# Kernel optimization log

Hardware: AMD Instinct MI355X
Metric: run time of the kernel (lower is better)

Reference implementation:

```python
import jax, jax.numpy as jnp
import numpy as np

SR = 44100.0
N_FFT = 2048
BANDS = 128
C_IN = 2
D_OUT = 128
B = 8
T = 512


def _hz_to_mel(f):
    # Slaney mel scale (librosa default, htk=False)
    f = np.asarray(f, dtype=np.float64)
    f_sp = 200.0 / 3.0
    min_log_hz = 1000.0
    min_log_mel = min_log_hz / f_sp  # 15.0
    logstep = np.log(6.4) / 27.0
    lin = f / f_sp
    log = min_log_mel + np.log(np.maximum(f, 1e-10) / min_log_hz) / logstep
    return np.where(f >= min_log_hz, log, lin)


def _mel_to_hz(m):
    m = np.asarray(m, dtype=np.float64)
    f_sp = 200.0 / 3.0
    min_log_mel = 15.0
    logstep = np.log(6.4) / 27.0
    lin = m * f_sp
    log = 1000.0 * np.exp(logstep * (m - min_log_mel))
    return np.where(m >= min_log_mel, log, lin)


def _mel_filters(sr, n_fft, n_mels):
    # librosa.filters.mel(..., norm=None, fmin=0, fmax=sr/2)
    F = n_fft // 2 + 1
    fftfreqs = np.linspace(0.0, sr / 2.0, F)
    mels = np.linspace(_hz_to_mel(0.0), _hz_to_mel(sr / 2.0), n_mels + 2)
    mel_f = _mel_to_hz(mels)
    fdiff = np.diff(mel_f)
    ramps = mel_f[:, None] - fftfreqs[None, :]
    lower = -ramps[:-2] / fdiff[:-1, None]
    upper = ramps[2:] / fdiff[1:, None]
    return np.maximum(0.0, np.minimum(lower, upper))  # (n_mels, F)


def _build_bands(sr, n_fft, bands_num):
    # Mirrors BandSplit.__init__: edge residual bands + per-band nonzero gather tables.
    F = n_fft // 2 + 1
    mb = _mel_filters(sr, n_fft, bands_num - 2)
    b0 = np.zeros(F)
    i = int(np.argmax(mb[0]))
    b0[:i] = 1.0 - mb[0, :i]
    bl = np.zeros(F)
    i = int(np.argmax(mb[-1]))
    bl[i:] = 1.0 - mb[-1, i:]
    melbanks = np.concatenate([b0[None, :], mb, bl[None, :]], axis=0)  # (K, F)
    ola = melbanks.sum(axis=0)  # (F,), ~1.0 everywhere
    idx_list = [np.nonzero(melbanks[k])[0] for k in range(bands_num)]
    W = max(len(ix) for ix in idx_list)  # max band width
    pad_idx = n_fft // 2
    idxs = np.full((bands_num, W), pad_idx, dtype=np.int32)
    vals = np.zeros((bands_num, W), dtype=np.float32)
    for k, ix in enumerate(idx_list):
        idxs[k, : len(ix)] = ix
        vals[k, : len(ix)] = melbanks[k, ix]
    mask = (vals != 0.0).astype(np.float32)
    return (idxs.reshape(-1), vals.reshape(-1), mask.reshape(-1),
            ola.astype(np.float32), W)


def setup_inputs() -> dict:
    key = jax.random.key(0)
    k_x, k_w1, k_b1, k_w2, k_b2 = jax.random.split(key, 5)
    idx_flat, mel_flat, mask_flat, ola, W = _build_bands(SR, N_FFT, BANDS)
    F = N_FFT // 2 + 1
    x = jax.random.normal(k_x, (B, C_IN, T, F), dtype=jnp.float32)
    i1 = W * C_IN
    bound1 = 1.0 / np.sqrt(i1)
    pre_w = jax.random.uniform(k_w1, (BANDS, i1, D_OUT), jnp.float32, -bound1, bound1)
    pre_b = jax.random.normal(k_b1, (BANDS, D_OUT), jnp.float32) * 0.01
    bound2 = 1.0 / np.sqrt(D_OUT)
    post_w = jax.random.uniform(k_w2, (BANDS, D_OUT, i1), jnp.float32, -bound2, bound2)
    post_b = jax.random.normal(k_b2, (BANDS, i1), jnp.float32) * 0.01
    return {
        "x": x,
        "pre_w": pre_w, "pre_b": pre_b,
        "post_w": post_w, "post_b": post_b,
        "mel_flat": jnp.asarray(mel_flat),
        "mask_flat": jnp.asarray(mask_flat),
        "ola_window": jnp.asarray(ola),
        "idx_flat": jnp.asarray(idx_flat),
    }


def reference(x, pre_w, pre_b, post_w, post_b, mel_flat, mask_flat, ola_window, idx_flat):
    Bn, C, Tn, Fq = x.shape
    K = pre_b.shape[0]
    W = pre_w.shape[1] // C
    # ---- transform: gather + mel weighting + per-band linear ----
    g = x[:, :, :, idx_flat] * (mel_flat * mask_flat)            # (b, c, t, K*W)
    g = g.reshape(Bn, C, Tn, K, W)                               # b c t k w
    g = g.transpose(0, 2, 3, 4, 1).reshape(Bn, Tn, K, W * C)     # b t k (w c)
    z = jnp.einsum('btki,kio->btko', g, pre_w) + pre_b           # (b, t, K, d)
    # ---- inverse_transform: per-band linear + masked scatter-add + OLA norm ----
    y = jnp.einsum('btkd,kdo->btko', z, post_w) + post_b         # (b, t, K, W*C)
    y = y.reshape(Bn, Tn, K, W, C)
    y = y.transpose(0, 4, 1, 2, 3).reshape(Bn, C, Tn, K * W)     # b c t (k w)
    y = y * mask_flat
    buf = jnp.zeros((Bn, C, Tn, Fq), dtype=x.dtype)
    buf = buf.at[:, :, :, idx_flat].add(y)                       # scatter_add over f
    return buf / ola_window
```

## Files before the change

### kernel.cpp

```cpp
#include <hip/hip_runtime.h>
#include <hip/hip_fp16.h>

typedef __attribute__((ext_vector_type(8))) short short8;
typedef __attribute__((ext_vector_type(4))) float f32x4;

#define TPB 256
constexpr int D_OUTC = 128;
constexpr int T_LEN  = 512;
constexpr int C_INC  = 2;
constexpr int F_BINS = 1025;
constexpr int N_BANDS= 128;
constexpr int MAX_W  = 80;
constexpr int SCAP   = 4224;

__device__ inline short8 cvt8(const float v[8]) {
  short8 h;
  #pragma unroll
  for (int j = 0; j < 8; ++j) {
    unsigned u = __float_as_uint(v[j]);
    unsigned r = u + 0x7FFFu + ((u >> 16) & 1u);
    h[j] = (short)(r >> 16);
  }
  return h;
}

__global__ void k_len(const float* __restrict__ mask, const int* __restrict__ idx, int W,
                      int* __restrict__ lenT, int* __restrict__ startT) {
  const int k = blockIdx.x;
  const int lane = threadIdx.x;
  int cnt = 0;
  for (int w = lane; w < W; w += 64) cnt += (mask[k * W + w] != 0.f) ? 1 : 0;
  #pragma unroll
  for (int s = 32; s > 0; s >>= 1) cnt += __shfl_xor(cnt, s, 64);
  if (lane == 0) { lenT[k] = cnt; startT[k] = idx[k * W]; }
}
__global__ void k_scan(const int* __restrict__ lenT, int* __restrict__ lenPT,
                       int* __restrict__ offT, int* __restrict__ permT) {
  const int k = threadIdx.x;
  int l = lenT[k];
  lenPT[k] = (l + 15) & ~15;
  __shared__ int sh[N_BANDS];
  __shared__ int sl[N_BANDS];
  sh[k] = 2 * l;
  sl[k] = l;
  __syncthreads();
  for (int s = 1; s < N_BANDS; s <<= 1) {
    int t = (k >= s) ? sh[k - s] : 0;
    __syncthreads();
    sh[k] += t;
    __syncthreads();
  }
  offT[k] = sh[k] - 2 * l;
  if (k == N_BANDS - 1) offT[N_BANDS] = sh[k];
  int rank = 0;
  for (int j = 0; j < N_BANDS; ++j)
    rank += (sl[j] > l) || (sl[j] == l && j < k);
  permT[rank] = k;
}

__global__ void prep_w1(const float* __restrict__ pre_w, const float* __restrict__ mel,
                        const float* __restrict__ mask, const int* __restrict__ lenPT,
                        unsigned short* __restrict__ hh,
                        int W, int i1, int K1PA) {
  const int band = blockIdx.y;
  const int ip = blockIdx.x * 32 + (threadIdx.x & 31);
  const int lp = lenPT[band];
  const int c  = (ip >= lp) ? 1 : 0;
  const int w  = ip - (c ? lp : 0);
  const bool live = (ip < 2 * lp) && (w < W);
  float s = 0.f; int row = 0;
  if (live) { s = mel[band * W + w] * mask[band * W + w]; row = 2 * w + c; }
  for (int d = (threadIdx.x >> 5); d < D_OUTC; d += 8) {
    float v = live ? s * pre_w[((size_t)band * i1 + row) * D_OUTC + d] : 0.f;
    unsigned u = __float_as_uint(v);
    unsigned r = u + 0x7FFFu + ((u >> 16) & 1u);
    hh[((size_t)(band * D_OUTC + d)) * K1PA + ip] = (unsigned short)(r >> 16);
  }
}

__global__ void prep_w2(const float* __restrict__ post_w, const float* __restrict__ post_b,
                        const float* __restrict__ mask,
                        const int* __restrict__ idx, const float* __restrict__ ola,
                        unsigned short* __restrict__ hh, float* __restrict__ postbS,
                        int W, int i1, int K1PA) {
  const int band = blockIdx.y;
  const int o  = blockIdx.x * 2 + (threadIdx.x >> 7);
  const int dd = threadIdx.x & 127;
  float s = 0.f;
  if (o < i1) {
    int w = o >> 1;
    float mk = mask[band * W + w];
    if (mk != 0.f) s = mk / ola[idx[band * W + w]];
  }
  float v = (o < i1) ? s * post_w[((size_t)band * D_OUTC + dd) * i1 + o] : 0.f;
  unsigned u = __float_as_uint(v);
  unsigned r = u + 0x7FFFu + ((u >> 16) & 1u);
  hh[((size_t)(band * K1PA + o)) * D_OUTC + dd] = (unsigned short)(r >> 16);
  if (dd == 0 && o < i1)
    postbS[band * i1 + o] = s * post_b[band * i1 + o];
}

__global__ void k_inv2(const int* __restrict__ startT, const int* __restrict__ lenT,
                       const int* __restrict__ offT, int* __restrict__ inv) {
  int f = blockIdx.x * 256 + threadIdx.x;
  if (f >= F_BINS) return;
  int r0 = -1, r1 = -1, r2 = -1, r3 = -1;
  int n = 0;
  for (int k = 0; k < N_BANDS; ++k) {
    unsigned rel = (unsigned)(f - startT[k]);
    if (rel < (unsigned)lenT[k]) {
      int v = offT[k] + 2 * (int)rel;
      if (n == 0) r0 = v; else if (n == 1) r1 = v; else if (n == 2) r2 = v; else if (n == 3) r3 = v;
      ++n;
    }
  }
  *(int4*)&inv[f * 4] = make_int4(r0, r1, r2, r3);
}

__global__ __launch_bounds__(TPB, 4)
void bandsplit_main(const float* __restrict__ x,
                    const unsigned short* __restrict__ wB1h,
                    const unsigned short* __restrict__ wB2h,
                    const float* __restrict__ pre_b,
                    const float* __restrict__ postbS,
                    const int* __restrict__ lenT,
                    const int* __restrict__ lenPT,
                    const int* __restrict__ offT,
                    const int* __restrict__ startT,
                    const int* __restrict__ permT,
                    __half* __restrict__ y,
                    int i1, int K1PA, int nmt)
{
  const int bid  = blockIdx.x;
  const int band = permT[bid / nmt];
  const int mt   = bid - (bid / nmt) * nmt;

  const int lenv = lenT[band];
  if (lenv == 0) return;
  const int lp   = lenPT[band];
  const int nks  = lp >> 4;
  const int i1e  = 2 * lenv;
  const int nOT  = (i1e + 15) >> 4;
  const int offk = offT[band];
  const int strt = startT[band];

  const int mbase = mt * 128;
  const int b  = mbase >> 9;
  const int t0 = mbase & 511;
  const int tid  = threadIdx.x;
  const int lane = tid & 63;
  const int wid  = tid >> 6;
  const int lr = lane & 15, lk = lane >> 4;
  const int m0 = wid * 32;

  __shared__ float zAll[4][16 * 132];
  float* zw = zAll[wid];

  const float* xr0A = x + ((size_t)(b * C_INC) * T_LEN + (t0 + m0 + lr)) * F_BINS + strt;
  const float* xr0B = xr0A + (size_t)16 * F_BINS;
  const size_t xcs = (size_t)T_LEN * F_BINS;

  f32x4 a1A[8] = {}, a1B[8] = {};
  const unsigned short* b1h = wB1h + ((size_t)(band * D_OUTC) + lr) * K1PA;

  for (int ks = 0; ks < nks; ++ks) {
    const int i0 = ks * 32 + lk * 8;
    const int cs = (i0 >= lp) ? 1 : 0;
    const int w0 = i0 - (cs ? lp : 0);
    const float* xrA = xr0A + (cs ? xcs : 0) + w0;
    const float* xrB = xr0B + (cs ? xcs : 0) + w0;
    float xvA[8], xvB[8];
    if (w0 + 8 <= lenv) {
      float4 q0, q1, q2, q3;
      __builtin_memcpy(&q0, xrA,     16);
      __builtin_memcpy(&q1, xrA + 4, 16);
      __builtin_memcpy(&q2, xrB,     16);
      __builtin_memcpy(&q3, xrB + 4, 16);
      xvA[0]=q0.x; xvA[1]=q0.y; xvA[2]=q0.z; xvA[3]=q0.w;
      xvA[4]=q1.x; xvA[5]=q1.y; xvA[6]=q1.z; xvA[7]=q1.w;
      xvB[0]=q2.x; xvB[1]=q2.y; xvB[2]=q2.z; xvB[3]=q2.w;
      xvB[4]=q3.x; xvB[5]=q3.y; xvB[6]=q3.z; xvB[7]=q3.w;
    } else {
      #pragma unroll
      for (int j = 0; j < 8; ++j) {
        bool ok = (w0 + j < lenv);
        xvA[j] = ok ? xrA[j] : 0.f;
        xvB[j] = ok ? xrB[j] : 0.f;
      }
    }
    const short8 ahA = cvt8(xvA);
    const short8 ahB = cvt8(xvB);

    #pragma unroll
    for (int half = 0; half < 2; ++half) {
      short8 BH[4];
      #pragma unroll
      for (int t = 0; t < 4; ++t) {
        const int dt = half * 4 + t;
        BH[t] = *(const short8*)&b1h[(size_t)dt * 16 * K1PA + i0];
      }
      #pragma unroll
      for (int t = 0; t < 4; ++t) {
        const int dt = half * 4 + t;
        a1A[dt] = __builtin_amdgcn_mfma_f32_16x16x32_bf16(ahA, BH[t], a1A[dt], 0, 0, 0);
        a1B[dt] = __builtin_amdgcn_mfma_f32_16x16x32_bf16(ahB, BH[t], a1B[dt], 0, 0, 0);
      }
    }
  }

  float pbv[8];
  #pragma unroll
  for (int dt = 0; dt < 8; ++dt) pbv[dt] = pre_b[band * D_OUTC + dt * 16 + lr];

  short8 zhA[4], zhB[4];
  #pragma unroll
  for (int dt = 0; dt < 8; ++dt)
    #pragma unroll
    for (int r = 0; r < 4; ++r)
      zw[(lk * 4 + r) * 132 + dt * 16 + lr] = a1A[dt][r] + pbv[dt];
  __syncthreads();
  #pragma unroll
  for (int ks = 0; ks < 4; ++ks) {
    float zv[8];
    *(float4*)&zv[0] = *(const float4*)&zw[lr * 132 + ks * 32 + lk * 8];
    *(float4*)&zv[4] = *(const float4*)&zw[lr * 132 + ks * 32 + lk * 8 + 4];
    zhA[ks] = cvt8(zv);
  }
  __syncthreads();
  #pragma unroll
  for (int dt = 0; dt < 8; ++dt)
    #pragma unroll
    for (int r = 0; r < 4; ++r)
      zw[(lk * 4 + r) * 132 + dt * 16 + lr] = a1B[dt][r] + pbv[dt];
  __syncthreads();
  #pragma unroll
  for (int ks = 0; ks < 4; ++ks) {
    float zv[8];
    *(float4*)&zv[0] = *(const float4*)&zw[lr * 132 + ks * 32 + lk * 8];
    *(float4*)&zv[4] = *(const float4*)&zw[lr * 132 + ks * 32 + lk * 8 + 4];
    zhB[ks] = cvt8(zv);
  }

  const unsigned short* b2h = wB2h + ((size_t)(band * K1PA) + lr) * D_OUTC;
  for (int ot = 0; ot < nOT; ot += 2) {
    const bool has2 = (ot + 1 < nOT);
    short8 B0[4], B1[4];
    #pragma unroll
    for (int ks = 0; ks < 4; ++ks)
      B0[ks] = *(const short8*)&b2h[(size_t)ot * 16 * D_OUTC + ks * 32 + lk * 8];
    if (has2) {
      #pragma unroll
      for (int ks = 0; ks < 4; ++ks)
        B1[ks] = *(const short8*)&b2h[(size_t)(ot + 1) * 16 * D_OUTC + ks * 32 + lk * 8];
    }
    f32x4 aA0 = {}, aB0 = {}, aA1 = {}, aB1 = {};
    #pragma unroll
    for (int ks = 0; ks < 4; ++ks) {
      aA0 = __builtin_amdgcn_mfma_f32_16x16x32_bf16(zhA[ks], B0[ks], aA0, 0, 0, 0);
      aB0 = __builtin_amdgcn_mfma_f32_16x16x32_bf16(zhB[ks], B0[ks], aB0, 0, 0, 0);
    }
    if (has2) {
      #pragma unroll
      for (int ks = 0; ks < 4; ++ks) {
        aA1 = __builtin_amdgcn_mfma_f32_16x16x32_bf16(zhA[ks], B1[ks], aA1, 0, 0, 0);
        aB1 = __builtin_amdgcn_mfma_f32_16x16x32_bf16(zhB[ks], B1[ks], aB1, 0, 0, 0);
      }
    }
    {
      const int o = ot * 16 + lr;
      if (o < i1e) {
        const float pb = postbS[band * i1 + o];
        const size_t ybA = ((size_t)(b * T_LEN + t0 + m0 + lk * 4)) * SCAP + offk + o;
        const size_t ybB = ybA + (size_t)16 * SCAP;
        #pragma unroll
        for (int r = 0; r < 4; ++r) {
          y[ybA + (size_t)r * SCAP] = __float2half_rn(aA0[r] + pb);
          y[ybB + (size_t)r * SCAP] = __float2half_rn(aB0[r] + pb);
        }
      }
    }
    if (has2) {
      const int o = (ot + 1) * 16 + lr;
      if (o < i1e) {
        const float pb = postbS[band * i1 + o];
        const size_t ybA = ((size_t)(b * T_LEN + t0 + m0 + lk * 4)) * SCAP + offk + o;
        const size_t ybB = ybA + (size_t)16 * SCAP;
        #pragma unroll
        for (int r = 0; r < 4; ++r) {
          y[ybA + (size_t)r * SCAP] = __float2half_rn(aA1[r] + pb);
          y[ybB + (size_t)r * SCAP] = __float2half_rn(aB1[r] + pb);
        }
      }
    }
  }
}

__global__ __launch_bounds__(256, 8)
void k_merge(const __half* __restrict__ y, const int* __restrict__ inv,
             float* __restrict__ out, int nrows) {
  for (int row = blockIdx.x; row < nrows; row += gridDim.x) {
    const int t  = row & 511;
    const int bc = row >> 9;
    const int c  = bc & 1;
    const int b  = bc >> 1;
    const size_t ybase = (size_t)(b * T_LEN + t) * SCAP + c;
    float* orow = out + (size_t)row * F_BINS;
    for (int f = threadIdx.x; f < F_BINS; f += 256) {
      const int4 iv = *reinterpret_cast<const int4*>(&inv[f * 4]);
      float s = 0.f;
      if (iv.x >= 0) s += __half2float(y[ybase + iv.x]);
      if (iv.y >= 0) s += __half2float(y[ybase + iv.y]);
      if (iv.z >= 0) s += __half2float(y[ybase + iv.z]);
      if (iv.w >= 0) s += __half2float(y[ybase + iv.w]);
      orow[f] = s;
    }
  }
}

constexpr int MT     = 32;
constexpr int MAX_I1 = 2 * MAX_W;
constexpr int MAX_I1P= (MAX_I1 + 31) & ~31;
constexpr int GSTR   = 36;

__global__ __launch_bounds__(TPB, 2)
void bandsplit_fused(const float* __restrict__ x,
                     const float* __restrict__ pre_w,
                     const float* __restrict__ pre_b,
                     const float* __restrict__ post_w,
                     const float* __restrict__ post_b,
                     const float* __restrict__ mel,
                     const float* __restrict__ mask,
                     const float* __restrict__ ola,
                     const int*   __restrict__ idx,
                     float* __restrict__ out,
                     int W)
{
    const int i1  = 2 * W;
    const int I1P = (i1 + 31) & ~31;
    const int k     = blockIdx.y;
    const int mbase = blockIdx.x * MT;
    const int b     = mbase / T_LEN;
    const int t0    = mbase % T_LEN;
    const int tid = threadIdx.x;
    const int td  = tid & 31;
    const int tm  = tid >> 5;

    __shared__ float gT[MAX_I1P * GSTR];
    __shared__ float zT[D_OUTC * GSTR];
    __shared__ float wS[32 * D_OUTC];
    __shared__ float s_preb[D_OUTC];
    __shared__ float s_postb[MAX_I1];
    __shared__ float s_melmask[MAX_W];
    __shared__ float s_mask[MAX_W];
    __shared__ float s_iola[MAX_W];
    __shared__ int   s_idx[MAX_W];

    for (int j = tid; j < W; j += TPB) {
        int   f  = idx[k * W + j];
        float mv = mel[k * W + j];
        float mk = mask[k * W + j];
        s_idx[j]     = f;
        s_melmask[j] = mv * mk;
        s_mask[j]    = mk;
        s_iola[j]    = 1.0f / ola[f];
    }
    for (int j = tid; j < D_OUTC; j += TPB) s_preb[j]  = pre_b[k * D_OUTC + j];
    for (int j = tid; j < i1;     j += TPB) s_postb[j] = post_b[k * i1 + j];
    for (int j = tid; j < I1P * GSTR; j += TPB) gT[j] = 0.f;
    __syncthreads();

    for (int j = tid; j < MT * i1; j += TPB) {
        int w  = j % W;
        int cm = j / W;
        int c  = cm & 1;
        int ml = cm >> 1;
        int f  = s_idx[w];
        float v = x[((b * C_INC + c) * T_LEN + (t0 + ml)) * F_BINS + f] * s_melmask[w];
        gT[(2 * w + c) * GSTR + ml] = v;
    }
    __syncthreads();

    float az[4][4] = {};
    for (int i0 = 0; i0 < I1P; i0 += 32) {
        for (int j = tid; j < 32 * D_OUTC; j += TPB) {
            int ii = j >> 7, d = j & 127;
            int i  = i0 + ii;
            wS[j] = (i < i1) ? pre_w[(k * i1 + i) * D_OUTC + d] : 0.f;
        }
        __syncthreads();
        #pragma unroll 8
        for (int ii = 0; ii < 32; ++ii) {
            const float4 wv = *reinterpret_cast<const float4*>(&wS[ii * D_OUTC + td * 4]);
            const float4 gv = *reinterpret_cast<const float4*>(&gT[(i0 + ii) * GSTR + tm * 4]);
            az[0][0] += gv.x * wv.x; az[0][1] += gv.x * wv.y; az[0][2] += gv.x * wv.z; az[0][3] += gv.x * wv.w;
            az[1][0] += gv.y * wv.x; az[1][1] += gv.y * wv.y; az[1][2] += gv.y * wv.z; az[1][3] += gv.y * wv.w;
            az[2][0] += gv.z * wv.x; az[2][1] += gv.z * wv.y; az[2][2] += gv.z * wv.z; az[2][3] += gv.z * wv.w;
            az[3][0] += gv.w * wv.x; az[3][1] += gv.w * wv.y; az[3][2] += gv.w * wv.z; az[3][3] += gv.w * wv.w;
        }
        __syncthreads();
    }
    #pragma unroll
    for (int jj = 0; jj < 4; ++jj) {
        int d = td * 4 + jj;
        float bb = s_preb[d];
        #pragma unroll
        for (int r = 0; r < 4; ++r)
            zT[d * GSTR + tm * 4 + r] = az[r][jj] + bb;
    }
    __syncthreads();

    const int NOG = (i1 + 127) >> 7;
    for (int og = 0; og < NOG; ++og) {
        float ay[4][4] = {};
        for (int d0 = 0; d0 < D_OUTC; d0 += 32) {
            for (int j = tid; j < 32 * D_OUTC; j += TPB) {
                int dd = j >> 7, oo = j & 127;
                int o  = og * 128 + oo;
                wS[j] = (o < i1) ? post_w[(k * D_OUTC + d0 + dd) * i1 + o] : 0.f;
            }
            __syncthreads();
            #pragma unroll 8
            for (int dd = 0; dd < 32; ++dd) {
                const float4 wv = *reinterpret_cast<const float4*>(&wS[dd * D_OUTC + td * 4]);
                const float4 zv = *reinterpret_cast<const float4*>(&zT[(d0 + dd) * GSTR + tm * 4]);
                ay[0][0] += zv.x * wv.x; ay[0][1] += zv.x * wv.y; ay[0][2] += zv.x * wv.z; ay[0][3] += zv.x * wv.w;
                ay[1][0] += zv.y * wv.x; ay[1][1] += zv.y * wv.y; ay[1][2] += zv.y * wv.z; ay[1][3] += zv.y * wv.w;
                ay[2][0] += zv.z * wv.x; ay[2][1] += zv.z * wv.y; ay[2][2] += zv.z * wv.z; ay[2][3] += zv.z * wv.w;
                ay[3][0] += zv.w * wv.x; ay[3][1] += zv.w * wv.y; ay[3][2] += zv.w * wv.z; ay[3][3] += zv.w * wv.w;
            }
            __syncthreads();
        }
        #pragma unroll
        for (int jj = 0; jj < 4; ++jj) {
            int o = og * 128 + td * 4 + jj;
            if (o < i1) {
                int w = o >> 1, c = o & 1;
                float mk = s_mask[w];
                if (mk != 0.f) {
                    int f = s_idx[w];
                    float scale = mk * s_iola[w];
                    float bb = s_postb[o];
                    #pragma unroll
                    for (int r = 0; r < 4; ++r) {
                        int ml = tm * 4 + r;
                        float val = (ay[r][jj] + bb) * scale;
                        atomicAdd(&out[((b * C_INC + c) * T_LEN + (t0 + ml)) * F_BINS + f], val);
                    }
                }
            }
        }
    }
}

__global__ void bandsplit_naive(const float* __restrict__ x,
                                const float* __restrict__ pre_w,
                                const float* __restrict__ pre_b,
                                const float* __restrict__ post_w,
                                const float* __restrict__ post_b,
                                const float* __restrict__ mel,
                                const float* __restrict__ mask,
                                const float* __restrict__ ola,
                                const int*   __restrict__ idx,
                                float* __restrict__ out,
                                int W)
{
    const int i1 = 2 * W;
    extern __shared__ float sh[];
    float* g = sh;
    float* z = sh + i1;
    const int m = blockIdx.x, k = blockIdx.y;
    const int b = m / T_LEN, t = m % T_LEN;
    const int tid = threadIdx.x;
    for (int j = tid; j < i1; j += 128) {
        int w = j >> 1, c = j & 1;
        int f = idx[k * W + w];
        g[j] = x[((b * C_INC + c) * T_LEN + t) * F_BINS + f] * mel[k * W + w] * mask[k * W + w];
    }
    __syncthreads();
    {
        int d = tid;
        float a = pre_b[k * D_OUTC + d];
        for (int i = 0; i < i1; ++i) a += g[i] * pre_w[(k * i1 + i) * D_OUTC + d];
        z[d] = a;
    }
    __syncthreads();
    for (int o = tid; o < i1; o += 128) {
        int w = o >> 1, c = o & 1;
        float mk = mask[k * W + w];
        if (mk == 0.f) continue;
        float a = post_b[k * i1 + o];
        for (int d = 0; d < D_OUTC; ++d) a += z[d] * post_w[(k * D_OUTC + d) * i1 + o];
        int f = idx[k * W + w];
        atomicAdd(&out[((b * C_INC + c) * T_LEN + t) * F_BINS + f], a * mk / ola[f]);
    }
}

extern "C" void kernel_launch(void* const* d_in, const int* in_sizes, int n_in,
                              void* d_out, int out_size, void* d_ws, size_t ws_size,
                              hipStream_t stream) {
    const float* x      = (const float*)d_in[0];
    const float* pre_w  = (const float*)d_in[1];
    const float* pre_b  = (const float*)d_in[2];
    const float* post_w = (const float*)d_in[3];
    const float* post_b = (const float*)d_in[4];
    const float* mel    = (const float*)d_in[5];
    const float* mask   = (const float*)d_in[6];
    const float* ola    = (const float*)d_in[7];
    const int*   idxp   = (const int*)d_in[8];
    float* out = (float*)d_out;

    const int W  = in_sizes[8] / N_BANDS;
    const int i1 = 2 * W;
    const int Mrows = in_sizes[0] / (C_INC * F_BINS);
    const int K1PA = 2 * ((W + 15) & ~15);

    const size_t S1 = (size_t)N_BANDS * D_OUTC * K1PA;
    const size_t wbytes   = 4 * S1;
    const size_t pbs_off  = (wbytes + 15) & ~(size_t)15;
    const size_t inv_off  = (pbs_off + (size_t)N_BANDS * i1 * 4 + 15) & ~(size_t)15;
    const size_t len_off  = inv_off + (size_t)F_BINS * 4 * 4;
    const size_t lenp_off = len_off + N_BANDS * 4;
    const size_t offt_off = lenp_off + N_BANDS * 4;
    const size_t strt_off = offt_off + (N_BANDS + 1) * 4;
    const size_t perm_off = strt_off + N_BANDS * 4;
    const size_t y_off    = (perm_off + N_BANDS * 4 + 255) & ~(size_t)255;
    const size_t need     = y_off + (size_t)Mrows * SCAP * sizeof(__half);

    if (W <= MAX_W && (Mrows % 128) == 0 && (Mrows % T_LEN) == 0 && ws_size >= need) {
        char* ws = (char*)d_ws;
        unsigned short* wB1h = (unsigned short*)ws;
        unsigned short* wB2h = wB1h + S1;
        float* postbS = (float*)(ws + pbs_off);
        int* inv   = (int*)(ws + inv_off);
        int* lenT  = (int*)(ws + len_off);
        int* lenPT = (int*)(ws + lenp_off);
        int* offT  = (int*)(ws + offt_off);
        int* startT= (int*)(ws + strt_off);
        int* permT = (int*)(ws + perm_off);
        __half* y  = (__half*)(ws + y_off);

        k_len<<<N_BANDS, 64, 0, stream>>>(mask, idxp, W, lenT, startT);
        k_scan<<<1, N_BANDS, 0, stream>>>(lenT, lenPT, offT, permT);
        dim3 g1(K1PA / 32, N_BANDS);
        prep_w1<<<g1, 256, 0, stream>>>(pre_w, mel, mask, lenPT, wB1h, W, i1, K1PA);
        dim3 g2(K1PA / 2, N_BANDS);
        prep_w2<<<g2, 256, 0, stream>>>(post_w, post_b, mask, idxp, ola, wB2h, postbS,
                                        W, i1, K1PA);
        k_inv2<<<(F_BINS + 255) / 256, 256, 0, stream>>>(startT, lenT, offT, inv);
        const int nmt = Mrows / 128;
        bandsplit_main<<<nmt * N_BANDS, TPB, 0, stream>>>(x, wB1h, wB2h,
                                                 pre_b, postbS, lenT, lenPT, offT, startT,
                                                 permT, y, i1, K1PA, nmt);
        const int nrows = out_size / F_BINS;
        k_merge<<<4096, 256, 0, stream>>>(y, inv, out, nrows);
        return;
    }

    hipMemsetAsync(d_out, 0, (size_t)out_size * sizeof(float), stream);
    if (W <= MAX_W && (Mrows % MT) == 0) {
        dim3 grid(Mrows / MT, N_BANDS);
        bandsplit_fused<<<grid, TPB, 0, stream>>>(x, pre_w, pre_b, post_w, post_b,
                                                  mel, mask, ola, idxp, out, W);
    } else {
        dim3 grid(Mrows, N_BANDS);
        size_t shmem = (size_t)(2 * W + D_OUTC) * sizeof(float);
        bandsplit_naive<<<grid, 128, shmem, stream>>>(x, pre_w, pre_b, post_w, post_b,
                                                      mel, mask, ola, idxp, out, W);
    }
}
```

Measured before the change: 128.0 us.

## Merge metadata kernels, halve main tile to 64 rows, pair channels in merge

Folds the three metadata kernels (length, scan, inverse table) into one single-block kernel, removing two launches. Shrinks bandsplit_main from 256 to 128 threads with 64-row tiles, which doubles the grid and halves shared memory per block. Makes k_merge process both channels per (b,t) row, reading the interleaved c0/c1 halves as one half2 load and writing two output rows. The single-block metadata kernel serialises the inverse-table build onto one CU, and the smaller tiles give less reuse of weights per block.

Result: slower. 189.2 us (+47.9%).

```diff
diff --git a/kernel.cpp b/kernel.cpp
--- a/kernel.cpp
+++ b/kernel.cpp
@@ -4,7 +4,6 @@
 typedef __attribute__((ext_vector_type(8))) short short8;
 typedef __attribute__((ext_vector_type(4))) float f32x4;
 
-#define TPB 256
 constexpr int D_OUTC = 128;
 constexpr int T_LEN  = 512;
 constexpr int C_INC  = 2;
@@ -24,25 +23,22 @@
   return h;
 }
 
-__global__ void k_len(const float* __restrict__ mask, const int* __restrict__ idx, int W,
-                      int* __restrict__ lenT, int* __restrict__ startT) {
-  const int k = blockIdx.x;
-  const int lane = threadIdx.x;
-  int cnt = 0;
-  for (int w = lane; w < W; w += 64) cnt += (mask[k * W + w] != 0.f) ? 1 : 0;
-  #pragma unroll
-  for (int s = 32; s > 0; s >>= 1) cnt += __shfl_xor(cnt, s, 64);
-  if (lane == 0) { lenT[k] = cnt; startT[k] = idx[k * W]; }
-}
-__global__ void k_scan(const int* __restrict__ lenT, int* __restrict__ lenPT,
-                       int* __restrict__ offT, int* __restrict__ permT) {
+__global__ void k_meta(const float* __restrict__ mask, const int* __restrict__ idx, int W,
+                       int* __restrict__ lenT, int* __restrict__ lenPT,
+                       int* __restrict__ offT, int* __restrict__ startT,
+                       int* __restrict__ permT, int* __restrict__ inv) {
   const int k = threadIdx.x;
-  int l = lenT[k];
-  lenPT[k] = (l + 15) & ~15;
-  __shared__ int sh[N_BANDS];
-  __shared__ int sl[N_BANDS];
+  int l = 0;
+  for (int w = 0; w < W; ++w) l += (mask[k * W + w] != 0.f) ? 1 : 0;
+  const int st = idx[k * W];
+  lenT[k]   = l;
+  lenPT[k]  = (l + 15) & ~15;
+  startT[k] = st;
+
+  __shared__ int sh[N_BANDS], sl[N_BANDS], sst[N_BANDS], sof[N_BANDS];
   sh[k] = 2 * l;
   sl[k] = l;
+  sst[k] = st;
   __syncthreads();
   for (int s = 1; s < N_BANDS; s <<= 1) {
     int t = (k >= s) ? sh[k - s] : 0;
@@ -50,12 +46,28 @@
     sh[k] += t;
     __syncthreads();
   }
-  offT[k] = sh[k] - 2 * l;
+  const int off = sh[k] - 2 * l;
+  offT[k] = off;
+  sof[k] = off;
   if (k == N_BANDS - 1) offT[N_BANDS] = sh[k];
   int rank = 0;
   for (int j = 0; j < N_BANDS; ++j)
     rank += (sl[j] > l) || (sl[j] == l && j < k);
   permT[rank] = k;
+  __syncthreads();
+  for (int f = threadIdx.x; f < F_BINS; f += 128) {
+    int r0 = -1, r1 = -1, r2 = -1, r3 = -1;
+    int n = 0;
+    for (int kk = 0; kk < N_BANDS; ++kk) {
+      unsigned rel = (unsigned)(f - sst[kk]);
+      if (rel < (unsigned)sl[kk]) {
+        int v = sof[kk] + 2 * (int)rel;
+        if (n == 0) r0 = v; else if (n == 1) r1 = v; else if (n == 2) r2 = v; else r3 = v;
+        ++n;
+      }
+    }
+    *(int4*)&inv[f * 4] = make_int4(r0, r1, r2, r3);
+  }
 }
 
 __global__ void prep_w1(const float* __restrict__ pre_w, const float* __restrict__ mel,
@@ -100,24 +112,7 @@
     postbS[band * i1 + o] = s * post_b[band * i1 + o];
 }
 
-__global__ void k_inv2(const int* __restrict__ startT, const int* __restrict__ lenT,
-                       const int* __restrict__ offT, int* __restrict__ inv) {
-  int f = blockIdx.x * 256 + threadIdx.x;
-  if (f >= F_BINS) return;
-  int r0 = -1, r1 = -1, r2 = -1, r3 = -1;
-  int n = 0;
-  for (int k = 0; k < N_BANDS; ++k) {
-    unsigned rel = (unsigned)(f - startT[k]);
-    if (rel < (unsigned)lenT[k]) {
-      int v = offT[k] + 2 * (int)rel;
-      if (n == 0) r0 = v; else if (n == 1) r1 = v; else if (n == 2) r2 = v; else if (n == 3) r3 = v;
-      ++n;
-    }
-  }
-  *(int4*)&inv[f * 4] = make_int4(r0, r1, r2, r3);
-}
-
-__global__ __launch_bounds__(TPB, 4)
+__global__ __launch_bounds__(128, 4)
 void bandsplit_main(const float* __restrict__ x,
                     const unsigned short* __restrict__ wB1h,
                     const unsigned short* __restrict__ wB2h,
@@ -144,7 +139,7 @@
   const int offk = offT[band];
   const int strt = startT[band];
 
-  const int mbase = mt * 128;
+  const int mbase = mt * 64;
   const int b  = mbase >> 9;
   const int t0 = mbase & 511;
   const int tid  = threadIdx.x;
@@ -153,7 +148,7 @@
   const int lr = lane & 15, lk = lane >> 4;
   const int m0 = wid * 32;
 
-  __shared__ float zAll[4][16 * 132];
+  __shared__ float zAll[2][16 * 132];
   float* zw = zAll[wid];
 
   const float* xr0A = x + ((size_t)(b * C_INC) * T_LEN + (t0 + m0 + lr)) * F_BINS + strt;
@@ -297,26 +292,40 @@
 
 __global__ __launch_bounds__(256, 8)
 void k_merge(const __half* __restrict__ y, const int* __restrict__ inv,
-             float* __restrict__ out, int nrows) {
-  for (int row = blockIdx.x; row < nrows; row += gridDim.x) {
-    const int t  = row & 511;
-    const int bc = row >> 9;
-    const int c  = bc & 1;
-    const int b  = bc >> 1;
-    const size_t ybase = (size_t)(b * T_LEN + t) * SCAP + c;
-    float* orow = out + (size_t)row * F_BINS;
+             float* __restrict__ out, int nbt) {
+  const size_t crow = (size_t)T_LEN * F_BINS;
+  for (int row = blockIdx.x; row < nbt; row += gridDim.x) {
+    const int t = row & 511;
+    const int b = row >> 9;
+    const size_t ybase = (size_t)row * SCAP;
+    float* o0 = out + ((size_t)(b * C_INC) * T_LEN + t) * F_BINS;
+    float* o1 = o0 + crow;
     for (int f = threadIdx.x; f < F_BINS; f += 256) {
       const int4 iv = *reinterpret_cast<const int4*>(&inv[f * 4]);
-      float s = 0.f;
-      if (iv.x >= 0) s += __half2float(y[ybase + iv.x]);
-      if (iv.y >= 0) s += __half2float(y[ybase + iv.y]);
-      if (iv.z >= 0) s += __half2float(y[ybase + iv.z]);
-      if (iv.w >= 0) s += __half2float(y[ybase + iv.w]);
-      orow[f] = s;
-    }
-  }
-}
-
+      float s0 = 0.f, s1 = 0.f;
+      if (iv.x >= 0) {
+        const __half2 h = *reinterpret_cast<const __half2*>(&y[ybase + iv.x]);
+        s0 += __half2float(h.x); s1 += __half2float(h.y);
+      }
+      if (iv.y >= 0) {
+        const __half2 h = *reinterpret_cast<const __half2*>(&y[ybase + iv.y]);
+        s0 += __half2float(h.x); s1 += __half2float(h.y);
+      }
+      if (iv.z >= 0) {
+        const __half2 h = *reinterpret_cast<const __half2*>(&y[ybase + iv.z]);
+        s0 += __half2float(h.x); s1 += __half2float(h.y);
+      }
+      if (iv.w >= 0) {
+        const __half2 h = *reinterpret_cast<const __half2*>(&y[ybase + iv.w]);
+        s0 += __half2float(h.x); s1 += __half2float(h.y);
+      }
+      o0[f] = s0;
+      o1[f] = s1;
+    }
+  }
+}
+
+#define TPB 256
 constexpr int MT     = 32;
 constexpr int MAX_I1 = 2 * MAX_W;
 constexpr int MAX_I1P= (MAX_I1 + 31) & ~31;
@@ -526,7 +535,7 @@
     const size_t y_off    = (perm_off + N_BANDS * 4 + 255) & ~(size_t)255;
     const size_t need     = y_off + (size_t)Mrows * SCAP * sizeof(__half);
 
-    if (W <= MAX_W && (Mrows % 128) == 0 && (Mrows % T_LEN) == 0 && ws_size >= need) {
+    if (W <= MAX_W && (Mrows % 64) == 0 && (Mrows % T_LEN) == 0 && ws_size >= need) {
         char* ws = (char*)d_ws;
         unsigned short* wB1h = (unsigned short*)ws;
         unsigned short* wB2h = wB1h + S1;
@@ -539,20 +548,17 @@
         int* permT = (int*)(ws + perm_off);
         __half* y  = (__half*)(ws + y_off);
 
-        k_len<<<N_BANDS, 64, 0, stream>>>(mask, idxp, W, lenT, startT);
-        k_scan<<<1, N_BANDS, 0, stream>>>(lenT, lenPT, offT, permT);
+        k_meta<<<1, 128, 0, stream>>>(mask, idxp, W, lenT, lenPT, offT, startT, permT, inv);
         dim3 g1(K1PA / 32, N_BANDS);
         prep_w1<<<g1, 256, 0, stream>>>(pre_w, mel, mask, lenPT, wB1h, W, i1, K1PA);
         dim3 g2(K1PA / 2, N_BANDS);
         prep_w2<<<g2, 256, 0, stream>>>(post_w, post_b, mask, idxp, ola, wB2h, postbS,
                                         W, i1, K1PA);
-        k_inv2<<<(F_BINS + 255) / 256, 256, 0, stream>>>(startT, lenT, offT, inv);
-        const int nmt = Mrows / 128;
-        bandsplit_main<<<nmt * N_BANDS, TPB, 0, stream>>>(x, wB1h, wB2h,
+        const int nmt = Mrows / 64;
+        bandsplit_main<<<nmt * N_BANDS, 128, 0, stream>>>(x, wB1h, wB2h,
                                                  pre_b, postbS, lenT, lenPT, offT, startT,
                                                  permT, y, i1, K1PA, nmt);
-        const int nrows = out_size / F_BINS;
-        k_merge<<<4096, 256, 0, stream>>>(y, inv, out, nrows);
+        k_merge<<<4096, 256, 0, stream>>>(y, inv, out, Mrows);
         return;
     }
 
```
